# Performance work log

Measured on AMD Instinct MI355X. Metric: run time of the kernel, lower is better.

The kernel has to match this reference:

```python
import jax, jax.numpy as jnp
import numpy as np

B, S, P, J = 32, 128, 2, 17
DIN, DOUT, DRNN, DHID = 2, 3, 128, 256
N = P * J
DT = 0.1   # delta_t from init
K = 4      # Euler steps, hardcoded k=int(4) in source


def setup_inputs() -> dict:
    key = jax.random.key(0)
    ks = jax.random.split(key, 12)
    g = lambda k, sh, fan: (jax.random.normal(k, sh, jnp.float32) / np.sqrt(fan)).astype(jnp.float32)
    d = {}
    d['x2d'] = jax.random.normal(ks[0], (B, S, P, J, DIN), jnp.float32)
    d['mask'] = jax.random.randint(ks[1], (B, S, P, J, 1), 0, 2).astype(jnp.int32)
    # ODE MLP: DRNN -> DHID -> DHID -> DRNN (num_hidden=2 hidden layers, tanh)
    d['ode_w0'] = g(ks[2], (DRNN, DHID), DRNN); d['ode_b0'] = jnp.zeros((DHID,), jnp.float32)
    d['ode_w1'] = g(ks[3], (DHID, DHID), DHID); d['ode_b1'] = jnp.zeros((DHID,), jnp.float32)
    d['ode_w2'] = g(ks[4], (DHID, DRNN), DHID); d['ode_b2'] = jnp.zeros((DRNN,), jnp.float32)
    # GRU cell 0: input DIN -> hidden DRNN ; GRU cell 1: input DRNN -> hidden DRNN
    d['wih0'] = g(ks[5], (DIN, 3 * DRNN), DIN);  d['whh0'] = g(ks[6], (DRNN, 3 * DRNN), DRNN)
    d['bih0'] = jnp.zeros((3 * DRNN,), jnp.float32); d['bhh0'] = jnp.zeros((3 * DRNN,), jnp.float32)
    d['wih1'] = g(ks[7], (DRNN, 3 * DRNN), DRNN); d['whh1'] = g(ks[8], (DRNN, 3 * DRNN), DRNN)
    d['bih1'] = jnp.zeros((3 * DRNN,), jnp.float32); d['bhh1'] = jnp.zeros((3 * DRNN,), jnp.float32)
    d['wout'] = g(ks[9], (DRNN, DOUT), DRNN); d['bout'] = jnp.zeros((DOUT,), jnp.float32)
    d['h0'] = 0.01 * jax.random.normal(ks[10], (1, 1, DRNN), jnp.float32)
    return d


def _ode(h, w0, b0, w1, b1, w2, b2):
    h = jnp.tanh(h @ w0 + b0)
    h = jnp.tanh(h @ w1 + b1)
    return h @ w2 + b2


def _gru(x, h, wih, whh, bih, bhh):
    gi = x @ wih + bih
    gh = h @ whh + bhh
    ir, iz, ig = jnp.split(gi, 3, axis=-1)
    hr, hz, hg = jnp.split(gh, 3, axis=-1)
    r = jax.nn.sigmoid(ir + hr)
    z = jax.nn.sigmoid(iz + hz)
    n = jnp.tanh(ig + r * hg)
    return (1.0 - z) * n + z * h


def reference(x2d, mask, ode_w0, ode_b0, ode_w1, ode_b1, ode_w2, ode_b2,
              wih0, whh0, bih0, bhh0, wih1, whh1, bih1, bhh1, wout, bout, h0):
    m = mask.astype(x2d.dtype)                      # (B,S,P,J,1)
    xs = (x2d * m).reshape(B, S, N, DIN)            # masked 2D input
    ms = m.reshape(B, S, N, 1)
    h_init = jnp.broadcast_to(h0, (B, N, DRNN))

    def step(h, inp):
        x, mm = inp                                 # (B,N,DIN), (B,N,1)
        h1 = h
        for _ in range(K):                          # 4 Euler ODE steps
            h1 = h1 + DT * _ode(h1, ode_w0, ode_b0, ode_w1, ode_b1, ode_w2, ode_b2)
        h2 = _gru(x, h1, wih0, whh0, bih0, bhh0)    # stacked GRU, both conditioned on h1
        h2 = _gru(h2, h1, wih1, whh1, bih1, bhh1)
        h_next = h1 * (1.0 - mm) + h2 * mm
        return h_next, h1

    _, hs = jax.lax.scan(step, h_init,
                         (jnp.swapaxes(xs, 0, 1), jnp.swapaxes(ms, 0, 1)))
    hs = jnp.swapaxes(hs, 0, 1)                     # (B,S,N,DRNN)
    ys = (hs @ wout + bout).reshape(B, S, P, J, DOUT)
    return ys
```

## Files before the change

### kernel.cpp

```cpp
#include <hip/hip_runtime.h>

typedef _Float16 f16x8 __attribute__((ext_vector_type(8)));
typedef float f32x4 __attribute__((ext_vector_type(4)));

constexpr int S_ = 128;
constexpr float DT_ = 0.1f;
constexpr float LS = 2048.0f;
constexpr float INV = 1.0f / 2048.0f;

#define MFMA(a, b, c) __builtin_amdgcn_mfma_f32_16x16x32_f16((a), (b), (c), 0, 0, 0)
#define SB() __builtin_amdgcn_sched_barrier(0)

#define OB0   0
#define OB1   256
#define OB2   512
#define OBHH0 640
#define OBIH0 1024
#define OBIH1 1408
#define OBHH1 1792
#define NBIAS 2176

__device__ __forceinline__ float fast_tanh(float x) {
    float e = __expf(2.0f * x);
    return 1.0f - 2.0f / (e + 1.0f);
}
__device__ __forceinline__ float fast_sigmoid(float x) {
    return 1.0f / (1.0f + __expf(-x));
}
__device__ __forceinline__ f32x4 bc4(float v) { return (f32x4){v, v, v, v}; }

__device__ __forceinline__ void gld16(const _Float16* g, _Float16* l) {
    __builtin_amdgcn_global_load_lds(
        (const __attribute__((address_space(1))) void*)g,
        (__attribute__((address_space(3))) void*)l, 16, 0, 0);
}
template<int N> __device__ __forceinline__ void waitvm() {
    if constexpr (N == 0) asm volatile("s_waitcnt vmcnt(0)" ::: "memory");
    else if constexpr (N == 2) asm volatile("s_waitcnt vmcnt(2)" ::: "memory");
    else if constexpr (N == 4) asm volatile("s_waitcnt vmcnt(4)" ::: "memory");
    SB();
}

__global__ void prep_hl(const float* __restrict__ src, _Float16* __restrict__ hi,
                        _Float16* __restrict__ lo, int K, int N) {
    int e = blockIdx.x * 256 + threadIdx.x;
    if (e >= K * N) return;
    int tile = e >> 9, r = e & 511;
    int lane = r >> 3, j = r & 7;
    int KT = K >> 5;
    int nt = tile / KT, kt = tile - nt * KT;
    int k = kt * 32 + ((lane >> 4) << 3) + j;
    int n = nt * 16 + (lane & 15);
    float v = src[k * N + n];
    _Float16 h = (_Float16)v;
    hi[e] = h;
    lo[e] = (_Float16)((v - (float)h) * LS);
}

template<int KT, int NTW>
__device__ __forceinline__ void mm_phase(
    const _Float16* __restrict__ Wh, const _Float16* __restrict__ Wl,
    const int* nts,
    const _Float16* __restrict__ Ah, const _Float16* __restrict__ Al, int lda,
    _Float16* wbase, int l, int lrow, int lk8,
    f32x4* acc, f32x4* pe, f32x4* qe)
{
    waitvm<0>();
    const int lb = l * 8;
#pragma unroll
    for (int t = 0; t < NTW; ++t) {
        gld16(Wh + ((size_t)nts[t] * KT) * 512 + lb, wbase + (2 * t) * 512);
        gld16(Wl + ((size_t)nts[t] * KT) * 512 + lb, wbase + (2 * t + 1) * 512);
    }
#pragma unroll
    for (int kt = 0; kt < KT; ++kt) {
        _Float16* cb = wbase + (kt & 1) * 2048;
        if (kt + 1 < KT) {
            SB();
            _Float16* nb = wbase + ((kt + 1) & 1) * 2048;
#pragma unroll
            for (int t = 0; t < NTW; ++t) {
                gld16(Wh + ((size_t)(nts[t] * KT + kt + 1)) * 512 + lb, nb + (2 * t) * 512);
                gld16(Wl + ((size_t)(nts[t] * KT + kt + 1)) * 512 + lb, nb + (2 * t + 1) * 512);
            }
            waitvm<2 * NTW>();
        } else {
            waitvm<0>();
        }
        f16x8 ah = *(const f16x8*)(Ah + lrow * lda + kt * 32 + lk8);
        f16x8 al = *(const f16x8*)(Al + lrow * lda + kt * 32 + lk8);
#pragma unroll
        for (int t = 0; t < NTW; ++t) {
            f16x8 bh = *(const f16x8*)(cb + (2 * t) * 512 + lb);
            f16x8 bl = *(const f16x8*)(cb + (2 * t + 1) * 512 + lb);
            acc[t] = MFMA(ah, bh, acc[t]);
            pe[t]  = MFMA(ah, bl, pe[t]);
            qe[t]  = MFMA(al, bh, qe[t]);
        }
    }
}

__global__ __launch_bounds__(512, 1) void odernn_mfma(
    const float* __restrict__ x2d, const int* __restrict__ maskp,
    const _Float16* __restrict__ w0h, const _Float16* __restrict__ w0l,
    const _Float16* __restrict__ w1hg, const _Float16* __restrict__ w1lg,
    const _Float16* __restrict__ w2h, const _Float16* __restrict__ w2l,
    const _Float16* __restrict__ hh0h, const _Float16* __restrict__ hh0l,
    const _Float16* __restrict__ ih1h, const _Float16* __restrict__ ih1l,
    const _Float16* __restrict__ hh1h, const _Float16* __restrict__ hh1l,
    const float* __restrict__ b0, const float* __restrict__ b1,
    const float* __restrict__ b2, const float* __restrict__ bhh0,
    const float* __restrict__ bih0, const float* __restrict__ wih0,
    const float* __restrict__ bih1, const float* __restrict__ bhh1,
    const float* __restrict__ wout, const float* __restrict__ bout,
    const float* __restrict__ h0, float* __restrict__ out)
{
    __shared__ float hF[16][128];
    __shared__ _Float16 bAh[16][264], bAl[16][264];
    __shared__ _Float16 bBh[16][264], bBl[16][264];
    __shared__ _Float16 bHh[16][136], bHl[16][136];
    __shared__ _Float16 wstage[8][2][4][512];
    __shared__ float sbias[NBIAS];
    __shared__ float swi0[768];
    __shared__ float swout[384];
    __shared__ float sbout[4];
    __shared__ float sx0[16], sx1[16], smm[16];
    __shared__ int sIdx[16];

    const int tid = (int)threadIdx.x;
    const int wv = tid >> 6;
    const int l = tid & 63;
    const int lrow = l & 15;
    const int lk8 = (l >> 4) << 3;
    const int rbase = (l >> 4) << 2;
    _Float16* wb = &wstage[wv][0][0][0];

    for (int e = tid; e < 256; e += 512) { sbias[OB0 + e] = b0[e]; sbias[OB1 + e] = b1[e]; }
    for (int e = tid; e < 128; e += 512) sbias[OB2 + e] = b2[e];
    for (int e = tid; e < 384; e += 512) {
        sbias[OBHH0 + e] = bhh0[e];
        sbias[OBIH0 + e] = bih0[e];
        sbias[OBIH1 + e] = bih1[e];
        sbias[OBHH1 + e] = bhh1[e];
        swout[e] = wout[e];
    }
    for (int e = tid; e < 768; e += 512) swi0[e] = wih0[e];
    if (tid < 3) sbout[tid] = bout[tid];
    for (int e = tid; e < 2048; e += 512) {
        int row = e >> 7, col = e & 127;
        float v = h0[col];
        hF[row][col] = v;
        _Float16 hh = (_Float16)v;
        bHh[row][col] = hh;
        bHl[row][col] = (_Float16)((v - (float)hh) * LS);
    }
    if (tid < 16) {
        int grow = (int)blockIdx.x * 16 + tid;
        int bb = grow / 34, nn = grow - bb * 34;
        sIdx[tid] = bb * (S_ * 34) + nn;
    }
    __syncthreads();

    const int nts01[2] = {wv, wv + 8};
    const int nts2[1] = {wv + 16};
    const int ntsw[1] = {wv};

    for (int s = 0; s < S_; ++s) {
        if (tid < 16) {
            int idx = sIdx[tid] + s * 34;
            float fm = (float)maskp[idx];
            smm[tid] = fm;
            sx0[tid] = x2d[2 * idx] * fm;
            sx1[tid] = x2d[2 * idx + 1] * fm;
        }

        for (int it = 0; it < 4; ++it) {
            {
                f32x4 acc[2] = {bc4(sbias[OB0 + (wv << 4) + lrow]),
                                bc4(sbias[OB0 + ((wv + 8) << 4) + lrow])};
                f32x4 pe[2] = {bc4(0.f), bc4(0.f)}, qe[2] = {bc4(0.f), bc4(0.f)};
                mm_phase<4, 2>(w0h, w0l, nts01, &bHh[0][0], &bHl[0][0], 136,
                               wb, l, lrow, lk8, acc, pe, qe);
                const int n0 = wv << 4, n1 = (wv + 8) << 4;
#pragma unroll
                for (int r = 0; r < 4; ++r) {
                    int row = rbase + r;
                    float v0 = fast_tanh(acc[0][r] + (pe[0][r] + qe[0][r]) * INV);
                    float v1 = fast_tanh(acc[1][r] + (pe[1][r] + qe[1][r]) * INV);
                    _Float16 hh = (_Float16)v0;
                    bBh[row][n0 + lrow] = hh;
                    bBl[row][n0 + lrow] = (_Float16)((v0 - (float)hh) * LS);
                    hh = (_Float16)v1;
                    bBh[row][n1 + lrow] = hh;
                    bBl[row][n1 + lrow] = (_Float16)((v1 - (float)hh) * LS);
                }
            }
            __syncthreads();

            {
                f32x4 acc[2] = {bc4(sbias[OB1 + (wv << 4) + lrow]),
                                bc4(sbias[OB1 + ((wv + 8) << 4) + lrow])};
                f32x4 pe[2] = {bc4(0.f), bc4(0.f)}, qe[2] = {bc4(0.f), bc4(0.f)};
                mm_phase<8, 2>(w1hg, w1lg, nts01, &bBh[0][0], &bBl[0][0], 264,
                               wb, l, lrow, lk8, acc, pe, qe);
                const int n0 = wv << 4, n1 = (wv + 8) << 4;
#pragma unroll
                for (int r = 0; r < 4; ++r) {
                    int row = rbase + r;
                    float v0 = fast_tanh(acc[0][r] + (pe[0][r] + qe[0][r]) * INV);
                    float v1 = fast_tanh(acc[1][r] + (pe[1][r] + qe[1][r]) * INV);
                    _Float16 hh = (_Float16)v0;
                    bAh[row][n0 + lrow] = hh;
                    bAl[row][n0 + lrow] = (_Float16)((v0 - (float)hh) * LS);
                    hh = (_Float16)v1;
                    bAh[row][n1 + lrow] = hh;
                    bAl[row][n1 + lrow] = (_Float16)((v1 - (float)hh) * LS);
                }
            }
            __syncthreads();

            {
                f32x4 acc[1] = {bc4(sbias[OB2 + (wv << 4) + lrow])};
                f32x4 pe[1] = {bc4(0.f)}, qe[1] = {bc4(0.f)};
                mm_phase<8, 1>(w2h, w2l, ntsw, &bAh[0][0], &bAl[0][0], 264,
                               wb, l, lrow, lk8, acc, pe, qe);
#pragma unroll
                for (int r = 0; r < 4; ++r) {
                    int row = rbase + r, col = (wv << 4) + lrow;
                    float v = hF[row][col] + DT_ * (acc[0][r] + (pe[0][r] + qe[0][r]) * INV);
                    hF[row][col] = v;
                    _Float16 hh = (_Float16)v;
                    bHh[row][col] = hh;
                    bHl[row][col] = (_Float16)((v - (float)hh) * LS);
                }
            }
            __syncthreads();
        }

        {
            f32x4 acc[3] = {bc4(sbias[OBHH0 + (wv << 4) + lrow]),
                            bc4(sbias[OBHH0 + ((wv + 8) << 4) + lrow]),
                            bc4(sbias[OBHH0 + ((wv + 16) << 4) + lrow])};
            f32x4 pe[3] = {bc4(0.f), bc4(0.f), bc4(0.f)};
            f32x4 qe[3] = {bc4(0.f), bc4(0.f), bc4(0.f)};
            mm_phase<4, 2>(hh0h, hh0l, nts01, &bHh[0][0], &bHl[0][0], 136,
                           wb, l, lrow, lk8, acc, pe, qe);
            mm_phase<4, 1>(hh0h, hh0l, nts2, &bHh[0][0], &bHl[0][0], 136,
                           wb, l, lrow, lk8, acc + 2, pe + 2, qe + 2);
            {
                int yrow = wv + ((l >> 5) << 3);
                int ll = l & 31;
                int c0 = ll << 2;
                float4 hv = *(const float4*)&hF[yrow][c0];
                float y0 = hv.x * swout[c0 * 3] + hv.y * swout[(c0 + 1) * 3] +
                           hv.z * swout[(c0 + 2) * 3] + hv.w * swout[(c0 + 3) * 3];
                float y1 = hv.x * swout[c0 * 3 + 1] + hv.y * swout[(c0 + 1) * 3 + 1] +
                           hv.z * swout[(c0 + 2) * 3 + 1] + hv.w * swout[(c0 + 3) * 3 + 1];
                float y2 = hv.x * swout[c0 * 3 + 2] + hv.y * swout[(c0 + 1) * 3 + 2] +
                           hv.z * swout[(c0 + 2) * 3 + 2] + hv.w * swout[(c0 + 3) * 3 + 2];
#pragma unroll
                for (int m = 16; m >= 1; m >>= 1) {
                    y0 += __shfl_xor(y0, m, 64);
                    y1 += __shfl_xor(y1, m, 64);
                    y2 += __shfl_xor(y2, m, 64);
                }
                if (ll == 0) {
                    int idx = sIdx[yrow] + s * 34;
                    out[idx * 3 + 0] = y0 + sbout[0];
                    out[idx * 3 + 1] = y1 + sbout[1];
                    out[idx * 3 + 2] = y2 + sbout[2];
                }
            }
            {
                int col = (wv << 4) + lrow;
                float wxr0 = swi0[col], wxr1 = swi0[384 + col];
                float wxz0 = swi0[128 + col], wxz1 = swi0[384 + 128 + col];
                float wxn0 = swi0[256 + col], wxn1 = swi0[384 + 256 + col];
                float bir = sbias[OBIH0 + col], biz = sbias[OBIH0 + 128 + col], bin = sbias[OBIH0 + 256 + col];
#pragma unroll
                for (int r = 0; r < 4; ++r) {
                    int row = rbase + r;
                    float xa = sx0[row], xb = sx1[row];
                    float rg = fast_sigmoid(bir + xa * wxr0 + xb * wxr1 + acc[0][r] + (pe[0][r] + qe[0][r]) * INV);
                    float zg = fast_sigmoid(biz + xa * wxz0 + xb * wxz1 + acc[1][r] + (pe[1][r] + qe[1][r]) * INV);
                    float gn = acc[2][r] + (pe[2][r] + qe[2][r]) * INV;
                    float nn = fast_tanh(bin + xa * wxn0 + xb * wxn1 + rg * gn);
                    float h1 = hF[row][col];
                    float h2 = (1.0f - zg) * nn + zg * h1;
                    _Float16 hh = (_Float16)h2;
                    bBh[row][col] = hh;
                    bBl[row][col] = (_Float16)((h2 - (float)hh) * LS);
                }
            }
        }
        __syncthreads();

        {
            f32x4 aI[3] = {bc4(sbias[OBIH1 + (wv << 4) + lrow]),
                           bc4(sbias[OBIH1 + ((wv + 8) << 4) + lrow]),
                           bc4(sbias[OBIH1 + ((wv + 16) << 4) + lrow])};
            f32x4 pI[3] = {bc4(0.f), bc4(0.f), bc4(0.f)};
            f32x4 qI[3] = {bc4(0.f), bc4(0.f), bc4(0.f)};
            mm_phase<4, 2>(ih1h, ih1l, nts01, &bBh[0][0], &bBl[0][0], 264,
                           wb, l, lrow, lk8, aI, pI, qI);
            mm_phase<4, 1>(ih1h, ih1l, nts2, &bBh[0][0], &bBl[0][0], 264,
                           wb, l, lrow, lk8, aI + 2, pI + 2, qI + 2);
            f32x4 gi0 = aI[0] + (pI[0] + qI[0]) * INV;
            f32x4 gi1 = aI[1] + (pI[1] + qI[1]) * INV;
            f32x4 gi2 = aI[2] + (pI[2] + qI[2]) * INV;

            f32x4 aH[3] = {bc4(sbias[OBHH1 + (wv << 4) + lrow]),
                           bc4(sbias[OBHH1 + ((wv + 8) << 4) + lrow]),
                           bc4(sbias[OBHH1 + ((wv + 16) << 4) + lrow])};
            f32x4 pH[3] = {bc4(0.f), bc4(0.f), bc4(0.f)};
            f32x4 qH[3] = {bc4(0.f), bc4(0.f), bc4(0.f)};
            mm_phase<4, 2>(hh1h, hh1l, nts01, &bHh[0][0], &bHl[0][0], 136,
                           wb, l, lrow, lk8, aH, pH, qH);
            mm_phase<4, 1>(hh1h, hh1l, nts2, &bHh[0][0], &bHl[0][0], 136,
                           wb, l, lrow, lk8, aH + 2, pH + 2, qH + 2);

            __syncthreads();
#pragma unroll
            for (int r = 0; r < 4; ++r) {
                int row = rbase + r, col = (wv << 4) + lrow;
                float ghr = aH[0][r] + (pH[0][r] + qH[0][r]) * INV;
                float ghz = aH[1][r] + (pH[1][r] + qH[1][r]) * INV;
                float ghn = aH[2][r] + (pH[2][r] + qH[2][r]) * INV;
                float rg = fast_sigmoid(gi0[r] + ghr);
                float zg = fast_sigmoid(gi1[r] + ghz);
                float nn = fast_tanh(gi2[r] + rg * ghn);
                float h1 = hF[row][col];
                float h2 = (1.0f - zg) * nn + zg * h1;
                float v = (smm[row] != 0.0f) ? h2 : h1;
                hF[row][col] = v;
                _Float16 hh = (_Float16)v;
                bHh[row][col] = hh;
                bHl[row][col] = (_Float16)((v - (float)hh) * LS);
            }
        }
        __syncthreads();
    }
}

extern "C" void kernel_launch(void* const* d_in, const int* in_sizes, int n_in,
                              void* d_out, int out_size, void* d_ws, size_t ws_size,
                              hipStream_t stream) {
    const float* x2d  = (const float*)d_in[0];
    const int*   mask = (const int*)d_in[1];
    const float* w0   = (const float*)d_in[2];
    const float* b0   = (const float*)d_in[3];
    const float* w1   = (const float*)d_in[4];
    const float* b1   = (const float*)d_in[5];
    const float* w2   = (const float*)d_in[6];
    const float* b2   = (const float*)d_in[7];
    const float* wih0 = (const float*)d_in[8];
    const float* whh0 = (const float*)d_in[9];
    const float* bih0 = (const float*)d_in[10];
    const float* bhh0 = (const float*)d_in[11];
    const float* wih1 = (const float*)d_in[12];
    const float* whh1 = (const float*)d_in[13];
    const float* bih1 = (const float*)d_in[14];
    const float* bhh1 = (const float*)d_in[15];
    const float* wout = (const float*)d_in[16];
    const float* bout = (const float*)d_in[17];
    const float* h0   = (const float*)d_in[18];
    float* out = (float*)d_out;

    _Float16* base = (_Float16*)d_ws;
    _Float16* pw0h  = base;
    _Float16* pw1h  = base + 32768;
    _Float16* pw2h  = base + 98304;
    _Float16* ph0h  = base + 131072;
    _Float16* pi1h  = base + 180224;
    _Float16* ph1h  = base + 229376;
    _Float16* lobase = base + 278528;
    _Float16* pw0l  = lobase;
    _Float16* pw1l  = lobase + 32768;
    _Float16* pw2l  = lobase + 98304;
    _Float16* ph0l  = lobase + 131072;
    _Float16* pi1l  = lobase + 180224;
    _Float16* ph1l  = lobase + 229376;

    hipLaunchKernelGGL(prep_hl, dim3(128), dim3(256), 0, stream, w0,   pw0h, pw0l, 128, 256);
    hipLaunchKernelGGL(prep_hl, dim3(256), dim3(256), 0, stream, w1,   pw1h, pw1l, 256, 256);
    hipLaunchKernelGGL(prep_hl, dim3(128), dim3(256), 0, stream, w2,   pw2h, pw2l, 256, 128);
    hipLaunchKernelGGL(prep_hl, dim3(192), dim3(256), 0, stream, whh0, ph0h, ph0l, 128, 384);
    hipLaunchKernelGGL(prep_hl, dim3(192), dim3(256), 0, stream, wih1, pi1h, pi1l, 128, 384);
    hipLaunchKernelGGL(prep_hl, dim3(192), dim3(256), 0, stream, whh1, ph1h, ph1l, 128, 384);

    hipLaunchKernelGGL(odernn_mfma, dim3(68), dim3(512), 0, stream,
        x2d, mask, pw0h, pw0l, pw1h, pw1l, pw2h, pw2l,
        ph0h, ph0l, pi1h, pi1l, ph1h, ph1l,
        b0, b1, b2, bhh0, bih0, wih0, bih1, bhh1, wout, bout, h0, out);
}
```

Measured before the change: 7.287 ms.

## Double block to 16 waves and split ODE matmul tiles across waves

The block grows from 512 to 1024 threads. Each of the 16 waves now computes one 16-column tile in the first two ODE layers instead of two tiles per wave across 8 waves. Waves 8-15 sit out the third ODE layer and the GRU matmuls; during the whh0 phase they compute the output projection, which moves that work off the main waves. The per-wave weight staging buffer is resized to fit this, with GRU waves taking double-size slices. The change gives the serial recurrence more latency hiding and less work per wave, but leaves half the waves idle in later phases and adds register pressure at 1024 threads.

```diff
diff --git a/kernel.cpp b/kernel.cpp
--- a/kernel.cpp
+++ b/kernel.cpp
@@ -65,6 +65,7 @@
     _Float16* wbase, int l, int lrow, int lk8,
     f32x4* acc, f32x4* pe, f32x4* qe)
 {
+    constexpr int SLICE = NTW * 1024;
     waitvm<0>();
     const int lb = l * 8;
 #pragma unroll
@@ -74,10 +75,10 @@
     }
 #pragma unroll
     for (int kt = 0; kt < KT; ++kt) {
-        _Float16* cb = wbase + (kt & 1) * 2048;
+        _Float16* cb = wbase + (kt & 1) * SLICE;
         if (kt + 1 < KT) {
             SB();
-            _Float16* nb = wbase + ((kt + 1) & 1) * 2048;
+            _Float16* nb = wbase + ((kt + 1) & 1) * SLICE;
 #pragma unroll
             for (int t = 0; t < NTW; ++t) {
                 gld16(Wh + ((size_t)(nts[t] * KT + kt + 1)) * 512 + lb, nb + (2 * t) * 512);
@@ -100,7 +101,7 @@
     }
 }
 
-__global__ __launch_bounds__(512, 1) void odernn_mfma(
+__global__ __launch_bounds__(1024, 1) void odernn_mfma(
     const float* __restrict__ x2d, const int* __restrict__ maskp,
     const _Float16* __restrict__ w0h, const _Float16* __restrict__ w0l,
     const _Float16* __restrict__ w1hg, const _Float16* __restrict__ w1lg,
@@ -119,7 +120,7 @@
     __shared__ _Float16 bAh[16][264], bAl[16][264];
     __shared__ _Float16 bBh[16][264], bBl[16][264];
     __shared__ _Float16 bHh[16][136], bHl[16][136];
-    __shared__ _Float16 wstage[8][2][4][512];
+    __shared__ _Float16 wstage[16][2048];
     __shared__ float sbias[NBIAS];
     __shared__ float swi0[768];
     __shared__ float swout[384];
@@ -133,20 +134,21 @@
     const int lrow = l & 15;
     const int lk8 = (l >> 4) << 3;
     const int rbase = (l >> 4) << 2;
-    _Float16* wb = &wstage[wv][0][0][0];
-
-    for (int e = tid; e < 256; e += 512) { sbias[OB0 + e] = b0[e]; sbias[OB1 + e] = b1[e]; }
-    for (int e = tid; e < 128; e += 512) sbias[OB2 + e] = b2[e];
-    for (int e = tid; e < 384; e += 512) {
+    _Float16* wb1 = &wstage[0][0] + wv * 2048;
+    _Float16* wb2 = &wstage[0][0] + wv * 4096;
+
+    for (int e = tid; e < 256; e += 1024) { sbias[OB0 + e] = b0[e]; sbias[OB1 + e] = b1[e]; }
+    for (int e = tid; e < 128; e += 1024) sbias[OB2 + e] = b2[e];
+    for (int e = tid; e < 384; e += 1024) {
         sbias[OBHH0 + e] = bhh0[e];
         sbias[OBIH0 + e] = bih0[e];
         sbias[OBIH1 + e] = bih1[e];
         sbias[OBHH1 + e] = bhh1[e];
         swout[e] = wout[e];
     }
-    for (int e = tid; e < 768; e += 512) swi0[e] = wih0[e];
+    for (int e = tid; e < 768; e += 1024) swi0[e] = wih0[e];
     if (tid < 3) sbout[tid] = bout[tid];
-    for (int e = tid; e < 2048; e += 512) {
+    for (int e = tid; e < 2048; e += 1024) {
         int row = e >> 7, col = e & 127;
         float v = h0[col];
         hF[row][col] = v;
@@ -176,54 +178,44 @@
 
         for (int it = 0; it < 4; ++it) {
             {
-                f32x4 acc[2] = {bc4(sbias[OB0 + (wv << 4) + lrow]),
-                                bc4(sbias[OB0 + ((wv + 8) << 4) + lrow])};
-                f32x4 pe[2] = {bc4(0.f), bc4(0.f)}, qe[2] = {bc4(0.f), bc4(0.f)};
-                mm_phase<4, 2>(w0h, w0l, nts01, &bHh[0][0], &bHl[0][0], 136,
-                               wb, l, lrow, lk8, acc, pe, qe);
-                const int n0 = wv << 4, n1 = (wv + 8) << 4;
+                f32x4 acc[1] = {bc4(sbias[OB0 + (wv << 4) + lrow])};
+                f32x4 pe[1] = {bc4(0.f)}, qe[1] = {bc4(0.f)};
+                mm_phase<4, 1>(w0h, w0l, ntsw, &bHh[0][0], &bHl[0][0], 136,
+                               wb1, l, lrow, lk8, acc, pe, qe);
+                const int n0 = wv << 4;
 #pragma unroll
                 for (int r = 0; r < 4; ++r) {
                     int row = rbase + r;
                     float v0 = fast_tanh(acc[0][r] + (pe[0][r] + qe[0][r]) * INV);
-                    float v1 = fast_tanh(acc[1][r] + (pe[1][r] + qe[1][r]) * INV);
                     _Float16 hh = (_Float16)v0;
                     bBh[row][n0 + lrow] = hh;
                     bBl[row][n0 + lrow] = (_Float16)((v0 - (float)hh) * LS);
-                    hh = (_Float16)v1;
-                    bBh[row][n1 + lrow] = hh;
-                    bBl[row][n1 + lrow] = (_Float16)((v1 - (float)hh) * LS);
                 }
             }
             __syncthreads();
 
             {
-                f32x4 acc[2] = {bc4(sbias[OB1 + (wv << 4) + lrow]),
-                                bc4(sbias[OB1 + ((wv + 8) << 4) + lrow])};
-                f32x4 pe[2] = {bc4(0.f), bc4(0.f)}, qe[2] = {bc4(0.f), bc4(0.f)};
-                mm_phase<8, 2>(w1hg, w1lg, nts01, &bBh[0][0], &bBl[0][0], 264,
-                               wb, l, lrow, lk8, acc, pe, qe);
-                const int n0 = wv << 4, n1 = (wv + 8) << 4;
+                f32x4 acc[1] = {bc4(sbias[OB1 + (wv << 4) + lrow])};
+                f32x4 pe[1] = {bc4(0.f)}, qe[1] = {bc4(0.f)};
+                mm_phase<8, 1>(w1hg, w1lg, ntsw, &bBh[0][0], &bBl[0][0], 264,
+                               wb1, l, lrow, lk8, acc, pe, qe);
+                const int n0 = wv << 4;
 #pragma unroll
                 for (int r = 0; r < 4; ++r) {
                     int row = rbase + r;
                     float v0 = fast_tanh(acc[0][r] + (pe[0][r] + qe[0][r]) * INV);
-                    float v1 = fast_tanh(acc[1][r] + (pe[1][r] + qe[1][r]) * INV);
                     _Float16 hh = (_Float16)v0;
                     bAh[row][n0 + lrow] = hh;
                     bAl[row][n0 + lrow] = (_Float16)((v0 - (float)hh) * LS);
-                    hh = (_Float16)v1;
-                    bAh[row][n1 + lrow] = hh;
-                    bAl[row][n1 + lrow] = (_Float16)((v1 - (float)hh) * LS);
                 }
             }
             __syncthreads();
 
-            {
+            if (wv < 8) {
                 f32x4 acc[1] = {bc4(sbias[OB2 + (wv << 4) + lrow])};
                 f32x4 pe[1] = {bc4(0.f)}, qe[1] = {bc4(0.f)};
                 mm_phase<8, 1>(w2h, w2l, ntsw, &bAh[0][0], &bAl[0][0], 264,
-                               wb, l, lrow, lk8, acc, pe, qe);
+                               wb1, l, lrow, lk8, acc, pe, qe);
 #pragma unroll
                 for (int r = 0; r < 4; ++r) {
                     int row = rbase + r, col = (wv << 4) + lrow;
@@ -238,40 +230,41 @@
         }
 
         {
-            f32x4 acc[3] = {bc4(sbias[OBHH0 + (wv << 4) + lrow]),
-                            bc4(sbias[OBHH0 + ((wv + 8) << 4) + lrow]),
-                            bc4(sbias[OBHH0 + ((wv + 16) << 4) + lrow])};
-            f32x4 pe[3] = {bc4(0.f), bc4(0.f), bc4(0.f)};
-            f32x4 qe[3] = {bc4(0.f), bc4(0.f), bc4(0.f)};
-            mm_phase<4, 2>(hh0h, hh0l, nts01, &bHh[0][0], &bHl[0][0], 136,
-                           wb, l, lrow, lk8, acc, pe, qe);
-            mm_phase<4, 1>(hh0h, hh0l, nts2, &bHh[0][0], &bHl[0][0], 136,
-                           wb, l, lrow, lk8, acc + 2, pe + 2, qe + 2);
-            {
-                int yrow = wv + ((l >> 5) << 3);
-                int ll = l & 31;
-                int c0 = ll << 2;
-                float4 hv = *(const float4*)&hF[yrow][c0];
-                float y0 = hv.x * swout[c0 * 3] + hv.y * swout[(c0 + 1) * 3] +
-                           hv.z * swout[(c0 + 2) * 3] + hv.w * swout[(c0 + 3) * 3];
-                float y1 = hv.x * swout[c0 * 3 + 1] + hv.y * swout[(c0 + 1) * 3 + 1] +
-                           hv.z * swout[(c0 + 2) * 3 + 1] + hv.w * swout[(c0 + 3) * 3 + 1];
-                float y2 = hv.x * swout[c0 * 3 + 2] + hv.y * swout[(c0 + 1) * 3 + 2] +
-                           hv.z * swout[(c0 + 2) * 3 + 2] + hv.w * swout[(c0 + 3) * 3 + 2];
-#pragma unroll
-                for (int m = 16; m >= 1; m >>= 1) {
-                    y0 += __shfl_xor(y0, m, 64);
-                    y1 += __shfl_xor(y1, m, 64);
-                    y2 += __shfl_xor(y2, m, 64);
-                }
-                if (ll == 0) {
-                    int idx = sIdx[yrow] + s * 34;
-                    out[idx * 3 + 0] = y0 + sbout[0];
-                    out[idx * 3 + 1] = y1 + sbout[1];
-                    out[idx * 3 + 2] = y2 + sbout[2];
-                }
-            }
-            {
+            f32x4 acc[3], pe[3], qe[3];
+            if (wv < 8) {
+                acc[0] = bc4(sbias[OBHH0 + (wv << 4) + lrow]);
+                acc[1] = bc4(sbias[OBHH0 + ((wv + 8) << 4) + lrow]);
+                acc[2] = bc4(sbias[OBHH0 + ((wv + 16) << 4) + lrow]);
+                pe[0] = bc4(0.f); pe[1] = bc4(0.f); pe[2] = bc4(0.f);
+                qe[0] = bc4(0.f); qe[1] = bc4(0.f); qe[2] = bc4(0.f);
+                mm_phase<4, 2>(hh0h, hh0l, nts01, &bHh[0][0], &bHl[0][0], 136,
+                               wb2, l, lrow, lk8, acc, pe, qe);
+                mm_phase<4, 1>(hh0h, hh0l, nts2, &bHh[0][0], &bHl[0][0], 136,
+                               wb2, l, lrow, lk8, acc + 2, pe + 2, qe + 2);
+            } else {
+                int g = wv - 8;
+#pragma unroll
+                for (int rr = 0; rr < 2; ++rr) {
+                    int yrow = g * 2 + rr;
+                    float ha = hF[yrow][2 * l], hb = hF[yrow][2 * l + 1];
+                    float y0 = ha * swout[(2 * l) * 3 + 0] + hb * swout[(2 * l + 1) * 3 + 0];
+                    float y1 = ha * swout[(2 * l) * 3 + 1] + hb * swout[(2 * l + 1) * 3 + 1];
+                    float y2 = ha * swout[(2 * l) * 3 + 2] + hb * swout[(2 * l + 1) * 3 + 2];
+#pragma unroll
+                    for (int m = 32; m >= 1; m >>= 1) {
+                        y0 += __shfl_xor(y0, m, 64);
+                        y1 += __shfl_xor(y1, m, 64);
+                        y2 += __shfl_xor(y2, m, 64);
+                    }
+                    if (l == 0) {
+                        int idx = sIdx[yrow] + s * 34;
+                        out[idx * 3 + 0] = y0 + sbout[0];
+                        out[idx * 3 + 1] = y1 + sbout[1];
+                        out[idx * 3 + 2] = y2 + sbout[2];
+                    }
+                }
+            }
+            if (wv < 8) {
                 int col = (wv << 4) + lrow;
                 float wxr0 = swi0[col], wxr1 = swi0[384 + col];
                 float wxz0 = swi0[128 + col], wxz1 = swi0[384 + 128 + col];
@@ -296,46 +289,50 @@
         __syncthreads();
 
         {
-            f32x4 aI[3] = {bc4(sbias[OBIH1 + (wv << 4) + lrow]),
-                           bc4(sbias[OBIH1 + ((wv + 8) << 4) + lrow]),
-                           bc4(sbias[OBIH1 + ((wv + 16) << 4) + lrow])};
-            f32x4 pI[3] = {bc4(0.f), bc4(0.f), bc4(0.f)};
-            f32x4 qI[3] = {bc4(0.f), bc4(0.f), bc4(0.f)};
-            mm_phase<4, 2>(ih1h, ih1l, nts01, &bBh[0][0], &bBl[0][0], 264,
-                           wb, l, lrow, lk8, aI, pI, qI);
-            mm_phase<4, 1>(ih1h, ih1l, nts2, &bBh[0][0], &bBl[0][0], 264,
-                           wb, l, lrow, lk8, aI + 2, pI + 2, qI + 2);
-            f32x4 gi0 = aI[0] + (pI[0] + qI[0]) * INV;
-            f32x4 gi1 = aI[1] + (pI[1] + qI[1]) * INV;
-            f32x4 gi2 = aI[2] + (pI[2] + qI[2]) * INV;
-
-            f32x4 aH[3] = {bc4(sbias[OBHH1 + (wv << 4) + lrow]),
-                           bc4(sbias[OBHH1 + ((wv + 8) << 4) + lrow]),
-                           bc4(sbias[OBHH1 + ((wv + 16) << 4) + lrow])};
-            f32x4 pH[3] = {bc4(0.f), bc4(0.f), bc4(0.f)};
-            f32x4 qH[3] = {bc4(0.f), bc4(0.f), bc4(0.f)};
-            mm_phase<4, 2>(hh1h, hh1l, nts01, &bHh[0][0], &bHl[0][0], 136,
-                           wb, l, lrow, lk8, aH, pH, qH);
-            mm_phase<4, 1>(hh1h, hh1l, nts2, &bHh[0][0], &bHl[0][0], 136,
-                           wb, l, lrow, lk8, aH + 2, pH + 2, qH + 2);
-
+            f32x4 gi0, gi1, gi2, aH[3], pH[3], qH[3];
+            if (wv < 8) {
+                f32x4 aI[3] = {bc4(sbias[OBIH1 + (wv << 4) + lrow]),
+                               bc4(sbias[OBIH1 + ((wv + 8) << 4) + lrow]),
+                               bc4(sbias[OBIH1 + ((wv + 16) << 4) + lrow])};
+                f32x4 pI[3] = {bc4(0.f), bc4(0.f), bc4(0.f)};
+                f32x4 qI[3] = {bc4(0.f), bc4(0.f), bc4(0.f)};
+                mm_phase<4, 2>(ih1h, ih1l, nts01, &bBh[0][0], &bBl[0][0], 264,
+                               wb2, l, lrow, lk8, aI, pI, qI);
+                mm_phase<4, 1>(ih1h, ih1l, nts2, &bBh[0][0], &bBl[0][0], 264,
+                               wb2, l, lrow, lk8, aI + 2, pI + 2, qI + 2);
+                gi0 = aI[0] + (pI[0] + qI[0]) * INV;
+                gi1 = aI[1] + (pI[1] + qI[1]) * INV;
+                gi2 = aI[2] + (pI[2] + qI[2]) * INV;
+
+                aH[0] = bc4(sbias[OBHH1 + (wv << 4) + lrow]);
+                aH[1] = bc4(sbias[OBHH1 + ((wv + 8) << 4) + lrow]);
+                aH[2] = bc4(sbias[OBHH1 + ((wv + 16) << 4) + lrow]);
+                pH[0] = bc4(0.f); pH[1] = bc4(0.f); pH[2] = bc4(0.f);
+                qH[0] = bc4(0.f); qH[1] = bc4(0.f); qH[2] = bc4(0.f);
+                mm_phase<4, 2>(hh1h, hh1l, nts01, &bHh[0][0], &bHl[0][0], 136,
+                               wb2, l, lrow, lk8, aH, pH, qH);
+                mm_phase<4, 1>(hh1h, hh1l, nts2, &bHh[0][0], &bHl[0][0], 136,
+                               wb2, l, lrow, lk8, aH + 2, pH + 2, qH + 2);
+            }
             __syncthreads();
-#pragma unroll
-            for (int r = 0; r < 4; ++r) {
-                int row = rbase + r, col = (wv << 4) + lrow;
-                float ghr = aH[0][r] + (pH[0][r] + qH[0][r]) * INV;
-                float ghz = aH[1][r] + (pH[1][r] + qH[1][r]) * INV;
-                float ghn = aH[2][r] + (pH[2][r] + qH[2][r]) * INV;
-                float rg = fast_sigmoid(gi0[r] + ghr);
-                float zg = fast_sigmoid(gi1[r] + ghz);
-                float nn = fast_tanh(gi2[r] + rg * ghn);
-                float h1 = hF[row][col];
-                float h2 = (1.0f - zg) * nn + zg * h1;
-                float v = (smm[row] != 0.0f) ? h2 : h1;
-                hF[row][col] = v;
-                _Float16 hh = (_Float16)v;
-                bHh[row][col] = hh;
-                bHl[row][col] = (_Float16)((v - (float)hh) * LS);
+            if (wv < 8) {
+#pragma unroll
+                for (int r = 0; r < 4; ++r) {
+                    int row = rbase + r, col = (wv << 4) + lrow;
+                    float ghr = aH[0][r] + (pH[0][r] + qH[0][r]) * INV;
+                    float ghz = aH[1][r] + (pH[1][r] + qH[1][r]) * INV;
+                    float ghn = aH[2][r] + (pH[2][r] + qH[2][r]) * INV;
+                    float rg = fast_sigmoid(gi0[r] + ghr);
+                    float zg = fast_sigmoid(gi1[r] + ghz);
+                    float nn = fast_tanh(gi2[r] + rg * ghn);
+                    float h1 = hF[row][col];
+                    float h2 = (1.0f - zg) * nn + zg * h1;
+                    float v = (smm[row] != 0.0f) ? h2 : h1;
+                    hF[row][col] = v;
+                    _Float16 hh = (_Float16)v;
+                    bHh[row][col] = hh;
+                    bHl[row][col] = (_Float16)((v - (float)hh) * LS);
+                }
             }
         }
         __syncthreads();
@@ -388,7 +385,7 @@
     hipLaunchKernelGGL(prep_hl, dim3(192), dim3(256), 0, stream, wih1, pi1h, pi1l, 128, 384);
     hipLaunchKernelGGL(prep_hl, dim3(192), dim3(256), 0, stream, whh1, ph1h, ph1l, 128, 384);
 
-    hipLaunchKernelGGL(odernn_mfma, dim3(68), dim3(512), 0, stream,
+    hipLaunchKernelGGL(odernn_mfma, dim3(68), dim3(1024), 0, stream,
         x2d, mask, pw0h, pw0l, pw1h, pw1l, pw2h, pw2l,
         ph0h, ph0l, pi1h, pi1l, ph1h, ph1l,
         b0, b1, b2, bhh0, bih0, wih0, bih1, bhh1, wout, bout, h0, out);
```

Result: slower. 9.956 ms (+36.6%).
